# Performance work log

Measured on AMD Instinct MI355X. Metric: run time of the kernel, lower is better.

## Reference

```python
import jax, jax.numpy as jnp
import numpy as np

N_NODES = 100000


def gcn_conv(x, edge_index, W, b):
    """PyG GCNConv: add self-loops, symmetric deg^{-1/2} normalization,
    linear transform, scatter-add aggregation, then bias."""
    n = x.shape[0]
    loops = jnp.arange(n, dtype=edge_index.dtype)
    src = jnp.concatenate([edge_index[0], loops])  # [E+N]
    dst = jnp.concatenate([edge_index[1], loops])  # [E+N]
    # degree (with self-loops) of each target node
    deg = jax.ops.segment_sum(jnp.ones_like(dst, dtype=x.dtype), dst, num_segments=n)
    dinv = jnp.where(deg > 0, jax.lax.rsqrt(deg), 0.0)
    norm = dinv[src] * dinv[dst]  # [E+N]
    h = x @ W  # [N, out_dim] -- transform before aggregation
    msg = h[src] * norm[:, None]  # gather + normalize
    out = jax.ops.segment_sum(msg, dst, num_segments=n)  # scatter-add
    return out + b


def setup_inputs() -> dict:
    key = jax.random.key(0)
    ks = jax.random.split(key, 8)
    n, e, d_in, d_h = N_NODES, 1600000, 32, 64
    x = jax.random.normal(ks[0], (n, d_in), dtype=jnp.float32)
    edge_index = jax.random.randint(ks[1], (2, e), 0, n, dtype=jnp.int64)
    # Glorot-style init for GCN weights, uniform for linear layer
    W1 = jax.random.normal(ks[2], (d_in, d_h), dtype=jnp.float32) / np.sqrt(d_in)
    b1 = jnp.zeros((d_h,), dtype=jnp.float32)
    W2 = jax.random.normal(ks[3], (d_h, d_h), dtype=jnp.float32) / np.sqrt(d_h)
    b2 = jnp.zeros((d_h,), dtype=jnp.float32)
    Wo = jax.random.normal(ks[4], (d_h, 1), dtype=jnp.float32) / np.sqrt(d_h)
    bo = jnp.zeros((1,), dtype=jnp.float32)
    return {"x": x, "edge_index": edge_index, "W1": W1, "b1": b1,
            "W2": W2, "b2": b2, "Wo": Wo, "bo": bo}


def reference(x, edge_index, W1, b1, W2, b2, Wo, bo):
    h = jax.nn.relu(gcn_conv(x, edge_index, W1, b1))
    h = jax.nn.relu(gcn_conv(h, edge_index, W2, b2))
    logits = h @ Wo + bo  # [N, 1]
    return jax.nn.sigmoid(logits).squeeze(-1)  # [N]
```

## Files before the change

### kernel.cpp

```cpp
#include <hip/hip_runtime.h>

#define DH 64
#define DIN 32
#define BSH 8
#define BNODES 256
#define MAXB 1024
#define CAPSH 13
#define CAP (1 << CAPSH)

typedef unsigned short u16;
typedef unsigned int u32;
typedef float f32x2 __attribute__((ext_vector_type(2)));

__device__ __forceinline__ float bf2f(u16 u) {
    union { u32 i; float f; } x; x.i = ((u32)u) << 16; return x.f;
}
__device__ __forceinline__ u16 f2bf(float f) {
    union { float f; u32 i; } x; x.f = f;
    u32 r = x.i + 0x7fff + ((x.i >> 16) & 1);
    return (u16)(r >> 16);
}
__device__ __forceinline__ float bfl(u32 u) {
    union { u32 i; float f; } x; x.i = u << 16; return x.f;
}
__device__ __forceinline__ float bfh(u32 u) {
    union { u32 i; float f; } x; x.i = u & 0xffff0000u; return x.f;
}
__device__ __forceinline__ void pkacc(f32x2& a, u32 u) {
    f32x2 b;
    b[0] = bfl(u); b[1] = bfh(u);
    asm("v_pk_add_f32 %0, %1, %0" : "+v"(a) : "v"(b));
}

__global__ void __launch_bounds__(512) binA_k(
        const int* __restrict__ ei, int* __restrict__ gcnt,
        u32* __restrict__ pairs, int E, int n, int nbuck) {
    __shared__ int lhist[MAXB];
    __shared__ int lbase[MAXB];
    __shared__ int smode;
    int t = threadIdx.x;
    if (t < 64) {
        int v = (2 * t + 1 < 2 * E) ? ei[2 * t + 1] : 0;
        unsigned long long b = __ballot(v != 0);
        if (t == 0) smode = (b != 0ULL) ? 1 : 0;
    }
    for (int b = t; b < nbuck; b += 512) lhist[b] = 0;
    __syncthreads();
    int m = smode;
    unsigned un = (unsigned)n;
    int q0 = blockIdx.x * 512 + t;
    int qs = gridDim.x * 512;

    if (m && !(E & 3)) {
        const int4* d4 = (const int4*)(ei + E);
        for (int q = q0; q < (E >> 2); q += qs) {
            int4 d = d4[q];
            if ((unsigned)d.x < un) atomicAdd(&lhist[d.x >> BSH], 1);
            if ((unsigned)d.y < un) atomicAdd(&lhist[d.y >> BSH], 1);
            if ((unsigned)d.z < un) atomicAdd(&lhist[d.z >> BSH], 1);
            if ((unsigned)d.w < un) atomicAdd(&lhist[d.w >> BSH], 1);
        }
    } else if (!m && !(E & 1)) {
        const int4* d4 = (const int4*)(ei + 2 * E);
        for (int q = q0; q < (E >> 1); q += qs) {
            int4 d = d4[q];
            if ((unsigned)d.x < un) atomicAdd(&lhist[d.x >> BSH], 1);
            if ((unsigned)d.z < un) atomicAdd(&lhist[d.z >> BSH], 1);
        }
    } else {
        const int* dstp = m ? (ei + E) : (ei + 2 * E);
        int stride = m ? 1 : 2;
        for (int e = q0; e < E; e += qs) {
            int d = dstp[(size_t)e * stride];
            if ((unsigned)d < un) atomicAdd(&lhist[d >> BSH], 1);
        }
    }
    __syncthreads();
    for (int b = t; b < nbuck; b += 512) {
        int c = lhist[b];
        lbase[b] = c ? ((b << CAPSH) + atomicAdd(&gcnt[b], c)) : 0;
        lhist[b] = 0;
    }
    __syncthreads();
    #define EMIT(S, D)                                                     \
        if ((unsigned)(D) < un) {                                          \
            int sv = ((unsigned)(S) < un) ? (S) : 0;                       \
            int bb = (D) >> BSH;                                           \
            int off = atomicAdd(&lhist[bb], 1);                            \
            int pos = lbase[bb] + off;                                     \
            if (pos < ((bb + 1) << CAPSH))                                 \
                pairs[pos] = ((u32)sv << BSH) | (u32)((D) & (BNODES - 1)); \
        }
    if (m && !(E & 3)) {
        const int4* s4 = (const int4*)ei;
        const int4* d4 = (const int4*)(ei + E);
        for (int q = q0; q < (E >> 2); q += qs) {
            int4 s = s4[q]; int4 d = d4[q];
            EMIT(s.x, d.x) EMIT(s.y, d.y) EMIT(s.z, d.z) EMIT(s.w, d.w)
        }
    } else if (!m && !(E & 1)) {
        const int4* s4 = (const int4*)ei;
        const int4* d4 = (const int4*)(ei + 2 * E);
        for (int q = q0; q < (E >> 1); q += qs) {
            int4 s = s4[q]; int4 d = d4[q];
            EMIT(s.x, d.x) EMIT(s.z, d.z)
        }
    } else {
        const int* srcp = ei;
        const int* dstp = m ? (ei + E) : (ei + 2 * E);
        int stride = m ? 1 : 2;
        for (int e = q0; e < E; e += qs) {
            int d = dstp[(size_t)e * stride];
            int s = srcp[(size_t)e * stride];
            EMIT(s, d)
        }
    }
    #undef EMIT
}

__global__ void __launch_bounds__(512) csr_build_k(
        const u32* __restrict__ pairs, const int* __restrict__ gcnt,
        int2* __restrict__ rse,
        int* __restrict__ col, float* __restrict__ dinv, int N) {
    __shared__ int cnt[BNODES];
    __shared__ int s[BNODES];
    int b = blockIdx.x, t = threadIdx.x;
    int base = b << CAPSH;
    int ec = gcnt[b]; if (ec > CAP) ec = CAP;
    int end = base + ec;
    if (t < BNODES) cnt[t] = 0;
    __syncthreads();
    for (int i = base + t; i < end; i += 512)
        atomicAdd(&cnt[pairs[i] & (BNODES - 1)], 1);
    __syncthreads();
    int v = (t < BNODES) ? cnt[t] : 0;
    if (t < BNODES) s[t] = v;
    __syncthreads();
    for (int off = 1; off < BNODES; off <<= 1) {
        int xsc = (t >= off && t < BNODES) ? s[t - off] : 0;
        __syncthreads();
        if (t < BNODES) s[t] += xsc;
        __syncthreads();
    }
    if (t < BNODES) {
        int excl = s[t] - v;
        int a = base + excl;
        int node = (b << BSH) + t;
        if (node < N) {
            rse[node]  = make_int2(a, a + v);
            dinv[node] = rsqrtf((float)v + 1.0f);
        }
        cnt[t] = a;
    }
    __syncthreads();
    for (int i = base + t; i < end; i += 512) {
        u32 p = pairs[i];
        int pos = atomicAdd(&cnt[p & (BNODES - 1)], 1);
        col[pos] = (int)((p >> BSH) << 7);
    }
}

__global__ void __launch_bounds__(256) gemm1_k(
        const float* __restrict__ x, const float* __restrict__ W1,
        const float* __restrict__ dinv, u16* __restrict__ hp, int N) {
    __shared__ float Wl[DIN * DH];
    __shared__ float xl[16][DIN + 4];
    int t = threadIdx.x;
    {
        const float4* Wv = (const float4*)W1;
        float4* Wd = (float4*)Wl;
        #pragma unroll
        for (int r = 0; r < 2; r++) Wd[t + 256 * r] = Wv[t + 256 * r];
    }
    if (blockIdx.x == 0 && t < 32)
        ((float*)(hp + (size_t)N * DH))[t] = 0.f;
    if (t < 128) {
        int row = t >> 3, ck = (t & 7) * 4;
        int node = blockIdx.x * 16 + row;
        float4 vx = {0.f, 0.f, 0.f, 0.f};
        if (node < N)
            vx = *(const float4*)&x[(size_t)node * DIN + ck];
        *(float4*)&xl[row][ck] = vx;
    }
    __syncthreads();
    int lane = t & 63, w = t >> 6;
    int g = lane >> 4, c = lane & 15;
    int nl = w * 4 + g;
    int node = blockIdx.x * 16 + nl;
    const float* xr = xl[nl];
    float4 acc = {0.f, 0.f, 0.f, 0.f};
    #pragma unroll
    for (int k = 0; k < DIN; k++) {
        float xv = xr[k];
        float4 wv = *(const float4*)&Wl[k * DH + c * 4];
        acc.x += xv * wv.x; acc.y += xv * wv.y; acc.z += xv * wv.z; acc.w += xv * wv.w;
    }
    if (node < N) {
        float di = dinv[node];
        ushort4 o;
        o.x = f2bf(acc.x * di); o.y = f2bf(acc.y * di);
        o.z = f2bf(acc.z * di); o.w = f2bf(acc.w * di);
        *(ushort4*)&hp[(size_t)node * DH + c * 4] = o;
    }
}

__device__ __forceinline__ void edge_sum8_db(const u16* __restrict__ hp,
                                             const int* __restrict__ colb,
                                             int start, int deg, int gl, int c,
                                             int sentb, f32x2* __restrict__ acc) {
    int dm = deg;
    dm = max(dm, __shfl_xor(dm, 8, 64));
    dm = max(dm, __shfl_xor(dm, 16, 64));
    dm = max(dm, __shfl_xor(dm, 32, 64));
    if (dm <= 0) return;
    const char* hpco = (const char*)hp + ((u32)c << 4);
    #define COLS(B) (((B) < dm && (B) + c < deg) ? colb[start + (B) + c] : sentb)
    #define ISSUE(V, CB)                                                     \
        { _Pragma("unroll") for (int j = 0; j < 8; j++) {                    \
              int s_ = __shfl((CB), gl | j, 64);                             \
              (V)[j] = *(const uint4*)(hpco + s_); } }
    #define ACCUM(V)                                                         \
        { _Pragma("unroll") for (int j = 0; j < 8; j++) {                    \
              pkacc(acc[0], (V)[j].x); pkacc(acc[1], (V)[j].y);              \
              pkacc(acc[2], (V)[j].z); pkacc(acc[3], (V)[j].w); } }
    uint4 va[8], vb[8];
    int cbA = COLS(0);
    ISSUE(va, cbA)
    int cbB = COLS(8);
    for (int base = 0; base < dm; base += 16) {
        bool hb = base + 8 < dm;
        if (hb) ISSUE(vb, cbB)
        int cbN1 = COLS(base + 16);
        ACCUM(va)
        if (base + 16 < dm) ISSUE(va, cbN1)
        int cbN2 = COLS(base + 24);
        if (hb) ACCUM(vb)
        cbB = cbN2;
    }
    #undef COLS
    #undef ISSUE
    #undef ACCUM
}

__global__ void __launch_bounds__(256) agg_gemm_k(
        const u16* __restrict__ hp, const int2* __restrict__ rse,
        const int* __restrict__ col,
        const float* __restrict__ dinv, const float* __restrict__ b1,
        const float* __restrict__ W2, u16* __restrict__ hp2, int N) {
    __shared__ float Wl[DH * DH];
    __shared__ float xs[4][8][DH + 4];
    int tid = threadIdx.x;
    {
        const float4* Wv = (const float4*)W2;
        float4* Wd = (float4*)Wl;
        #pragma unroll
        for (int r = 0; r < 4; r++) Wd[tid + 256 * r] = Wv[tid + 256 * r];
    }
    if (blockIdx.x == 0 && tid < 32)
        ((float*)(hp2 + (size_t)N * DH))[tid] = 0.f;
    __syncthreads();
    int lane = tid & 63, w = tid >> 6;
    int g = lane >> 3, c = lane & 7, gl = g << 3;
    int node = blockIdx.x * 32 + w * 8 + g;
    int start = 0, deg = 0;
    if (node < N) { int2 se = rse[node]; start = se.x; deg = se.y - se.x; }
    f32x2 acc[4] = {{0.f,0.f},{0.f,0.f},{0.f,0.f},{0.f,0.f}};
    edge_sum8_db(hp, col, start, deg, gl, c, N << 7, acc);
    float di = (node < N) ? dinv[node] : 0.f;
    float o0=0.f,o1=0.f,o2=0.f,o3=0.f,o4=0.f,o5=0.f,o6=0.f,o7=0.f;
    if (node < N) {
        uint4 sv = *(const uint4*)&hp[(size_t)node * DH + c * 8];
        float4 blo = *(const float4*)&b1[c * 8];
        float4 bhi = *(const float4*)&b1[c * 8 + 4];
        o0 = fmaxf((acc[0][0] + bfl(sv.x)) * di + blo.x, 0.f);
        o1 = fmaxf((acc[0][1] + bfh(sv.x)) * di + blo.y, 0.f);
        o2 = fmaxf((acc[1][0] + bfl(sv.y)) * di + blo.z, 0.f);
        o3 = fmaxf((acc[1][1] + bfh(sv.y)) * di + blo.w, 0.f);
        o4 = fmaxf((acc[2][0] + bfl(sv.z)) * di + bhi.x, 0.f);
        o5 = fmaxf((acc[2][1] + bfh(sv.z)) * di + bhi.y, 0.f);
        o6 = fmaxf((acc[3][0] + bfl(sv.w)) * di + bhi.z, 0.f);
        o7 = fmaxf((acc[3][1] + bfh(sv.w)) * di + bhi.w, 0.f);
    }
    *(float4*)&xs[w][g][c * 8]     = make_float4(o0, o1, o2, o3);
    *(float4*)&xs[w][g][c * 8 + 4] = make_float4(o4, o5, o6, o7);
    const float* xr = xs[w][g];
    float4 alo = {0.f,0.f,0.f,0.f}, ahi = {0.f,0.f,0.f,0.f};
    #pragma unroll
    for (int k4 = 0; k4 < DH / 4; k4++) {
        float4 xv4 = *(const float4*)&xr[k4 * 4];
        float xj[4] = {xv4.x, xv4.y, xv4.z, xv4.w};
        #pragma unroll
        for (int j = 0; j < 4; j++) {
            const float* wr = &Wl[(k4 * 4 + j) * DH + c * 8];
            float4 w0 = *(const float4*)wr;
            float4 w1 = *(const float4*)(wr + 4);
            float xv = xj[j];
            alo.x += xv * w0.x; alo.y += xv * w0.y; alo.z += xv * w0.z; alo.w += xv * w0.w;
            ahi.x += xv * w1.x; ahi.y += xv * w1.y; ahi.z += xv * w1.z; ahi.w += xv * w1.w;
        }
    }
    if (node < N) {
        uint4 po;
        po.x = (u32)f2bf(alo.x * di) | ((u32)f2bf(alo.y * di) << 16);
        po.y = (u32)f2bf(alo.z * di) | ((u32)f2bf(alo.w * di) << 16);
        po.z = (u32)f2bf(ahi.x * di) | ((u32)f2bf(ahi.y * di) << 16);
        po.w = (u32)f2bf(ahi.z * di) | ((u32)f2bf(ahi.w * di) << 16);
        *(uint4*)&hp2[(size_t)node * DH + c * 8] = po;
    }
}

__global__ void __launch_bounds__(256) agg_head_k(
        const u16* __restrict__ hp, const int2* __restrict__ rse,
        const int* __restrict__ col,
        const float* __restrict__ dinv, const float* __restrict__ bias,
        const float* __restrict__ Wo, const float* __restrict__ bo,
        float* __restrict__ y, int N) {
    int lane = threadIdx.x & 63;
    int g = lane >> 3, c = lane & 7, gl = g << 3;
    int node = blockIdx.x * 32 + (threadIdx.x >> 6) * 8 + g;
    int start = 0, deg = 0;
    if (node < N) { int2 se = rse[node]; start = se.x; deg = se.y - se.x; }
    f32x2 acc[4] = {{0.f,0.f},{0.f,0.f},{0.f,0.f},{0.f,0.f}};
    edge_sum8_db(hp, col, start, deg, gl, c, N << 7, acc);
    float t = 0.f;
    if (node < N) {
        uint4 sv = *(const uint4*)&hp[(size_t)node * DH + c * 8];
        float4 blo = *(const float4*)&bias[c * 8];
        float4 bhi = *(const float4*)&bias[c * 8 + 4];
        float4 wlo = *(const float4*)&Wo[c * 8];
        float4 whi = *(const float4*)&Wo[c * 8 + 4];
        float di = dinv[node];
        t = fmaxf((acc[0][0] + bfl(sv.x)) * di + blo.x, 0.f) * wlo.x
          + fmaxf((acc[0][1] + bfh(sv.x)) * di + blo.y, 0.f) * wlo.y
          + fmaxf((acc[1][0] + bfl(sv.y)) * di + blo.z, 0.f) * wlo.z
          + fmaxf((acc[1][1] + bfh(sv.y)) * di + blo.w, 0.f) * wlo.w
          + fmaxf((acc[2][0] + bfl(sv.z)) * di + bhi.x, 0.f) * whi.x
          + fmaxf((acc[2][1] + bfh(sv.z)) * di + bhi.y, 0.f) * whi.y
          + fmaxf((acc[3][0] + bfl(sv.w)) * di + bhi.z, 0.f) * whi.z
          + fmaxf((acc[3][1] + bfh(sv.w)) * di + bhi.w, 0.f) * whi.w;
    }
    t += __shfl_xor(t, 1, 64);
    t += __shfl_xor(t, 2, 64);
    t += __shfl_xor(t, 4, 64);
    if (c == 0 && node < N) {
        float z = t + bo[0];
        y[node] = 1.f / (1.f + __expf(-z));
    }
}

extern "C" void kernel_launch(void* const* d_in, const int* in_sizes, int n_in,
                              void* d_out, int out_size, void* d_ws, size_t ws_size,
                              hipStream_t stream) {
    const float* x  = (const float*)d_in[0];
    const int*   ei = (const int*)d_in[1];
    const float* W1 = (const float*)d_in[2];
    const float* b1 = (const float*)d_in[3];
    const float* W2 = (const float*)d_in[4];
    const float* b2 = (const float*)d_in[5];
    const float* Wo = (const float*)d_in[6];
    const float* bo = (const float*)d_in[7];
    float* y = (float*)d_out;

    int N = in_sizes[0] / DIN;
    int E = in_sizes[1] / 2;
    int nbuck = ((N - 1) >> BSH) + 1;

    char* ws = (char*)d_ws;
    size_t off = 0;
    auto alloc = [&](size_t bytes) { char* p = ws + off; off += (bytes + 255) & ~(size_t)255; return p; };
    int*   gcnt   = (int*)alloc(MAXB * 4);
    int2*  rse    = (int2*)alloc((size_t)N * 8);
    float* dinv   = (float*)alloc((size_t)N * 4);
    int*   col    = (int*)alloc(((size_t)nbuck << CAPSH) * 4);
    size_t pair_b = ((size_t)nbuck << CAPSH) * 4;
    size_t hp_b   = (size_t)N * DH * 2 + 256;
    char*  bufA   = (char*)alloc(pair_b > hp_b ? pair_b : hp_b);
    u16*   bufB   = (u16*)alloc(hp_b);
    u16*   hp    = (u16*)bufA;
    u32*   pairs = (u32*)bufA;

    hipMemsetAsync(gcnt, 0, (size_t)nbuck * 4, stream);
    binA_k<<<256, 512, 0, stream>>>(ei, gcnt, pairs, E, N, nbuck);
    csr_build_k<<<nbuck, 512, 0, stream>>>(pairs, gcnt, rse, col, dinv, N);
    gemm1_k<<<(N + 15) / 16, 256, 0, stream>>>(x, W1, dinv, hp, N);
    agg_gemm_k<<<(N + 31) / 32, 256, 0, stream>>>(hp, rse, col, dinv, b1, W2, bufB, N);
    agg_head_k<<<(N + 31) / 32, 256, 0, stream>>>(bufB, rse, col, dinv, b2, Wo, bo, y, N);
}
```

Baseline: 191.8 us.

## Use rolling software-pipelined gather in layer-1 aggregation and enlarge binning blocks

Replaces the double-buffered edge gather in agg_gemm_k with a rolling 8-register pipeline. Each slot's accumulate is interleaved with the load for the next chunk, and the next column indices are prefetched one chunk ahead, so gather latency is hidden without doubling register buffers. Separately, the binning kernel moves from 512 to 1024 threads per block, which gives more work per block and fewer global atomics per bucket. The larger block may reduce occupancy or raise shared-memory atomic contention.

```diff
diff --git a/kernel.cpp b/kernel.cpp
--- a/kernel.cpp
+++ b/kernel.cpp
@@ -32,7 +32,7 @@
     asm("v_pk_add_f32 %0, %1, %0" : "+v"(a) : "v"(b));
 }
 
-__global__ void __launch_bounds__(512) binA_k(
+__global__ void __launch_bounds__(1024) binA_k(
         const int* __restrict__ ei, int* __restrict__ gcnt,
         u32* __restrict__ pairs, int E, int n, int nbuck) {
     __shared__ int lhist[MAXB];
@@ -44,12 +44,12 @@
         unsigned long long b = __ballot(v != 0);
         if (t == 0) smode = (b != 0ULL) ? 1 : 0;
     }
-    for (int b = t; b < nbuck; b += 512) lhist[b] = 0;
+    for (int b = t; b < nbuck; b += 1024) lhist[b] = 0;
     __syncthreads();
     int m = smode;
     unsigned un = (unsigned)n;
-    int q0 = blockIdx.x * 512 + t;
-    int qs = gridDim.x * 512;
+    int q0 = blockIdx.x * 1024 + t;
+    int qs = gridDim.x * 1024;
 
     if (m && !(E & 3)) {
         const int4* d4 = (const int4*)(ei + E);
@@ -76,7 +76,7 @@
         }
     }
     __syncthreads();
-    for (int b = t; b < nbuck; b += 512) {
+    for (int b = t; b < nbuck; b += 1024) {
         int c = lhist[b];
         lbase[b] = c ? ((b << CAPSH) + atomicAdd(&gcnt[b], c)) : 0;
         lhist[b] = 0;
@@ -202,6 +202,71 @@
         o.z = f2bf(acc.z * di); o.w = f2bf(acc.w * di);
         *(ushort4*)&hp[(size_t)node * DH + c * 4] = o;
     }
+}
+
+__device__ __forceinline__ void edge_sum_roll8(const u16* __restrict__ hp,
+                                               const int* __restrict__ colb,
+                                               int start, int deg, int gl, int c,
+                                               int sentb, f32x2* __restrict__ acc) {
+    int dm = deg;
+    dm = max(dm, __shfl_xor(dm, 8, 64));
+    dm = max(dm, __shfl_xor(dm, 16, 64));
+    dm = max(dm, __shfl_xor(dm, 32, 64));
+    if (dm <= 0) return;
+    const char* hpco = (const char*)hp + ((u32)c << 4);
+    int nch = (dm + 7) >> 3;
+    uint4 v0, v1, v2, v3, v4, v5, v6, v7;
+    int cb = (c < deg) ? colb[start + c] : sentb;
+    {
+        int s;
+        s = __shfl(cb, gl | 0, 64); v0 = *(const uint4*)(hpco + s);
+        s = __shfl(cb, gl | 1, 64); v1 = *(const uint4*)(hpco + s);
+        s = __shfl(cb, gl | 2, 64); v2 = *(const uint4*)(hpco + s);
+        s = __shfl(cb, gl | 3, 64); v3 = *(const uint4*)(hpco + s);
+        s = __shfl(cb, gl | 4, 64); v4 = *(const uint4*)(hpco + s);
+        s = __shfl(cb, gl | 5, 64); v5 = *(const uint4*)(hpco + s);
+        s = __shfl(cb, gl | 6, 64); v6 = *(const uint4*)(hpco + s);
+        s = __shfl(cb, gl | 7, 64); v7 = *(const uint4*)(hpco + s);
+    }
+    int cbn = (8 + c < deg) ? colb[start + 8 + c] : sentb;
+    for (int ch = 1; ch < nch; ch++) {
+        int cbu = cbn;
+        int nb2 = (ch + 1) << 3;
+        cbn = (nb2 + c < deg) ? colb[start + nb2 + c] : sentb;
+        int s;
+        s = __shfl(cbu, gl | 0, 64);
+        pkacc(acc[0], v0.x); pkacc(acc[1], v0.y); pkacc(acc[2], v0.z); pkacc(acc[3], v0.w);
+        v0 = *(const uint4*)(hpco + s);
+        s = __shfl(cbu, gl | 1, 64);
+        pkacc(acc[0], v1.x); pkacc(acc[1], v1.y); pkacc(acc[2], v1.z); pkacc(acc[3], v1.w);
+        v1 = *(const uint4*)(hpco + s);
+        s = __shfl(cbu, gl | 2, 64);
+        pkacc(acc[0], v2.x); pkacc(acc[1], v2.y); pkacc(acc[2], v2.z); pkacc(acc[3], v2.w);
+        v2 = *(const uint4*)(hpco + s);
+        s = __shfl(cbu, gl | 3, 64);
+        pkacc(acc[0], v3.x); pkacc(acc[1], v3.y); pkacc(acc[2], v3.z); pkacc(acc[3], v3.w);
+        v3 = *(const uint4*)(hpco + s);
+        s = __shfl(cbu, gl | 4, 64);
+        pkacc(acc[0], v4.x); pkacc(acc[1], v4.y); pkacc(acc[2], v4.z); pkacc(acc[3], v4.w);
+        v4 = *(const uint4*)(hpco + s);
+        s = __shfl(cbu, gl | 5, 64);
+        pkacc(acc[0], v5.x); pkacc(acc[1], v5.y); pkacc(acc[2], v5.z); pkacc(acc[3], v5.w);
+        v5 = *(const uint4*)(hpco + s);
+        s = __shfl(cbu, gl | 6, 64);
+        pkacc(acc[0], v6.x); pkacc(acc[1], v6.y); pkacc(acc[2], v6.z); pkacc(acc[3], v6.w);
+        v6 = *(const uint4*)(hpco + s);
+        s = __shfl(cbu, gl | 7, 64);
+        pkacc(acc[0], v7.x); pkacc(acc[1], v7.y); pkacc(acc[2], v7.z); pkacc(acc[3], v7.w);
+        v7 = *(const uint4*)(hpco + s);
+    }
+    pkacc(acc[0], v0.x); pkacc(acc[1], v0.y); pkacc(acc[2], v0.z); pkacc(acc[3], v0.w);
+    pkacc(acc[0], v1.x); pkacc(acc[1], v1.y); pkacc(acc[2], v1.z); pkacc(acc[3], v1.w);
+    pkacc(acc[0], v2.x); pkacc(acc[1], v2.y); pkacc(acc[2], v2.z); pkacc(acc[3], v2.w);
+    pkacc(acc[0], v3.x); pkacc(acc[1], v3.y); pkacc(acc[2], v3.z); pkacc(acc[3], v3.w);
+    pkacc(acc[0], v4.x); pkacc(acc[1], v4.y); pkacc(acc[2], v4.z); pkacc(acc[3], v4.w);
+    pkacc(acc[0], v5.x); pkacc(acc[1], v5.y); pkacc(acc[2], v5.z); pkacc(acc[3], v5.w);
+    pkacc(acc[0], v6.x); pkacc(acc[1], v6.y); pkacc(acc[2], v6.z); pkacc(acc[3], v6.w);
+    pkacc(acc[0], v7.x); pkacc(acc[1], v7.y); pkacc(acc[2], v7.z); pkacc(acc[3], v7.w);
 }
 
 __device__ __forceinline__ void edge_sum8_db(const u16* __restrict__ hp,
@@ -265,7 +330,7 @@
     int start = 0, deg = 0;
     if (node < N) { int2 se = rse[node]; start = se.x; deg = se.y - se.x; }
     f32x2 acc[4] = {{0.f,0.f},{0.f,0.f},{0.f,0.f},{0.f,0.f}};
-    edge_sum8_db(hp, col, start, deg, gl, c, N << 7, acc);
+    edge_sum_roll8(hp, col, start, deg, gl, c, N << 7, acc);
     float di = (node < N) ? dinv[node] : 0.f;
     float o0=0.f,o1=0.f,o2=0.f,o3=0.f,o4=0.f,o5=0.f,o6=0.f,o7=0.f;
     if (node < N) {
@@ -380,7 +445,7 @@
     u32*   pairs = (u32*)bufA;
 
     hipMemsetAsync(gcnt, 0, (size_t)nbuck * 4, stream);
-    binA_k<<<256, 512, 0, stream>>>(ei, gcnt, pairs, E, N, nbuck);
+    binA_k<<<256, 1024, 0, stream>>>(ei, gcnt, pairs, E, N, nbuck);
     csr_build_k<<<nbuck, 512, 0, stream>>>(pairs, gcnt, rse, col, dinv, N);
     gemm1_k<<<(N + 15) / 16, 256, 0, stream>>>(x, W1, dinv, hp, N);
     agg_gemm_k<<<(N + 31) / 32, 256, 0, stream>>>(hp, rse, col, dinv, b1, W2, bufB, N);
```

Result: faster. 186.0 us (-3.0%).
